# Kernel tuning notes

Hardware: AMD Instinct MI355X
Metric: run time of the kernel (lower is better)

Reference implementation:

```python
import jax, jax.numpy as jnp
import numpy as np

N_NODES = 100000
N_EDGES = 3200000


def gcn_conv(x, W, b, src, dst, n_nodes):
    """PyG GCNConv: self-loops, symmetric D^-1/2 A D^-1/2 norm, linear, bias."""
    loop = jnp.arange(n_nodes, dtype=src.dtype)
    s = jnp.concatenate([src, loop])  # [E+N]
    d = jnp.concatenate([dst, loop])  # [E+N]
    # degree computed at destination (col), edge_weight = 1
    deg = jax.ops.segment_sum(jnp.ones_like(d, dtype=x.dtype), d,
                              num_segments=n_nodes)
    dinv = jnp.where(deg > 0, jax.lax.rsqrt(deg), 0.0)
    norm = dinv[s] * dinv[d]  # [E+N]
    h = x @ W.T  # [N, out]
    msg = h[s] * norm[:, None]  # gather + scale, [E+N, out]
    out = jax.ops.segment_sum(msg, d, num_segments=n_nodes)  # scatter-add
    return out + b


def setup_inputs() -> dict:
    key = jax.random.key(0)
    k1, k2, k3, k4 = jax.random.split(key, 4)
    x = jax.random.normal(k1, (N_NODES, 2), dtype=jnp.float32)
    edge_index = jax.random.randint(k2, (2, N_EDGES), 0, N_NODES,
                                    dtype=jnp.int64)
    # Glorot-ish init for linear weights
    W1 = jax.random.normal(k3, (64, 2), dtype=jnp.float32) * 0.5
    b1 = jnp.zeros((64,), dtype=jnp.float32)
    W2 = jax.random.normal(k4, (2, 64), dtype=jnp.float32) * 0.125
    b2 = jnp.zeros((2,), dtype=jnp.float32)
    return {"x": x, "edge_index": edge_index, "W1": W1, "b1": b1,
            "W2": W2, "b2": b2}


def reference(x, edge_index, W1, b1, W2, b2):
    src, dst = edge_index[0], edge_index[1]
    h = gcn_conv(x, W1, b1, src, dst, N_NODES)
    h = jax.nn.relu(h)
    out = gcn_conv(h, W2, b2, src, dst, N_NODES)
    return out
```

## Files before the change

kernel.cpp:

```cpp
#include <hip/hip_runtime.h>

#define N_NODES 100000
#define SHIFT 8
#define BNODES 256
#define NB 391
#define CAP 9728
#define TILE 8192
#define SB 1024


__global__ __launch_bounds__(SB, 8) void k_sort(const int* __restrict__ src,
                                                const int* __restrict__ dst,
                                                int* claim,
                                                const int* __restrict__ pz,
                                                int* sg, int e) {
    __shared__ int hist[2 * NB];
    __shared__ int rank[2 * NB];
    __shared__ int addrbase[NB];
    __shared__ int partials[16];
    __shared__ int stage[TILE];
    __shared__ unsigned short binmap[TILE];

    const int t = threadIdx.x;
    const int base = blockIdx.x * TILE;
    const int n = min(TILE, e - base);
    const int goff = (t >> 9) * NB;

    for (int i = t; i < 2 * NB; i += SB) hist[i] = 0;
    __syncthreads();

    int recs[8];
    int bins[8];
    int* myh = hist + goff;
#pragma unroll
    for (int k = 0; k < 2; ++k) {
        int idx = base + (k * SB + t) * 4;
        if (idx + 3 < e) {
            int4 s4 = *(const int4*)(src + idx);
            int4 d4 = *(const int4*)(dst + idx);
            int ss[4] = {s4.x, s4.y, s4.z, s4.w};
            int dd[4] = {d4.x, d4.y, d4.z, d4.w};
#pragma unroll
            for (int j = 0; j < 4; ++j) {
                int b = dd[j] >> SHIFT;
                bins[4 * k + j] = b;
                recs[4 * k + j] = ss[j] | ((dd[j] & (BNODES - 1)) << 17);
                atomicAdd(&myh[b], 1);
            }
        } else {
#pragma unroll
            for (int j = 0; j < 4; ++j) {
                int i2 = idx + j;
                if (i2 < e) {
                    int d = dst[i2];
                    int b = d >> SHIFT;
                    bins[4 * k + j] = b;
                    recs[4 * k + j] = src[i2] | ((d & (BNODES - 1)) << 17);
                    atomicAdd(&myh[b], 1);
                } else {
                    bins[4 * k + j] = -1;
                }
            }
        }
    }
    __syncthreads();

    int c0 = 0, c1 = 0, c = 0;
    if (t < NB) {
        c0 = hist[t];
        c1 = hist[NB + t];
        c = c0 + c1;
    }
    int vs = c;
#pragma unroll
    for (int off = 1; off < 64; off <<= 1) {
        int w = __shfl_up(vs, off, 64);
        if ((t & 63) >= off) vs += w;
    }
    if ((t & 63) == 63) partials[t >> 6] = vs;
    __syncthreads();
    int add = 0;
    for (int w = 0; w < (t >> 6); ++w) add += partials[w];
    vs += add;
    int excl = vs - c;
    const int P = *pz;
    if (t < NB) {
        rank[t] = excl;
        rank[NB + t] = excl + c0;
        int rb = c ? (atomicAdd(&claim[t], c) - P) : 0;
        addrbase[t] = t * CAP + rb - excl;
    }
    __syncthreads();

    int* myr = rank + goff;
#pragma unroll
    for (int m = 0; m < 8; ++m) {
        int b = bins[m];
        if (b >= 0) {
            int pos = atomicAdd(&myr[b], 1);
            stage[pos] = recs[m];
            binmap[pos] = (unsigned short)b;
        }
    }
    __syncthreads();

    for (int i = t; i < n; i += SB) {
        sg[addrbase[binmap[i]] + i] = stage[i];
    }
}

__global__ __launch_bounds__(1024) void k_refine(const int* __restrict__ claim,
                                                 const int* __restrict__ pz,
                                                 const int* __restrict__ sg,
                                                 const float* __restrict__ x,
                                                 int* sg2, int* packed,
                                                 float2* u) {
    __shared__ int hist[4 * BNODES];
    __shared__ int rank[4 * BNODES];
    __shared__ int partials[4];
    const int t = threadIdx.x;
    const int b = blockIdx.x;
    const int* p = sg + b * CAP;
    const int len = claim[b] - *pz;
    const int g = t >> 8;

    int4 r[3];
#pragma unroll
    for (int k = 0; k < 3; ++k) {
        int idx = 4 * t + 4096 * k;
        int4 v = make_int4(-1, -1, -1, -1);
        if (idx + 3 < len) v = *(const int4*)(p + idx);
        else if (idx < len) {
            v.x = p[idx];
            if (idx + 1 < len) v.y = p[idx + 1];
            if (idx + 2 < len) v.z = p[idx + 2];
        }
        r[k] = v;
    }
    for (int i = t; i < 4 * BNODES; i += 1024) hist[i] = 0;
    __syncthreads();
    int* myh = hist + g * BNODES;
#pragma unroll
    for (int k = 0; k < 3; ++k) {
        if (r[k].x != -1) atomicAdd(&myh[((unsigned)r[k].x) >> 17], 1);
        if (r[k].y != -1) atomicAdd(&myh[((unsigned)r[k].y) >> 17], 1);
        if (r[k].z != -1) atomicAdd(&myh[((unsigned)r[k].z) >> 17], 1);
        if (r[k].w != -1) atomicAdd(&myh[((unsigned)r[k].w) >> 17], 1);
    }
    __syncthreads();

    int c4x = 0, c4y = 0, c4z = 0, c4w = 0, tot = 0;
    if (t < BNODES) {
        c4x = hist[t];
        c4y = hist[BNODES + t];
        c4z = hist[2 * BNODES + t];
        c4w = hist[3 * BNODES + t];
        tot = (c4x + c4y) + (c4z + c4w);
    }
    int vs = tot;
#pragma unroll
    for (int off = 1; off < 64; off <<= 1) {
        int w = __shfl_up(vs, off, 64);
        if ((t & 63) >= off) vs += w;
    }
    if ((t & 63) == 63 && t < BNODES) partials[t >> 6] = vs;
    __syncthreads();
    if (t < BNODES) {
        int add = 0;
        for (int w = 0; w < (t >> 6); ++w) add += partials[w];
        vs += add;
        int excl = vs - tot;
        int run = excl;
        rank[t] = run; run += c4x;
        rank[BNODES + t] = run; run += c4y;
        rank[2 * BNODES + t] = run; run += c4z;
        rank[3 * BNODES + t] = run;
        int node = b * BNODES + t;
        if (node < N_NODES) {
            packed[node] = (b * CAP + excl) | (tot << 22);
            float dv = rsqrtf((float)(tot + 1));
            float2 xv = ((const float2*)x)[node];
            u[node] = make_float2(dv * xv.x, dv * xv.y);
        }
    }
    __syncthreads();

    int* q = sg2 + b * CAP;
    int* myr = rank + g * BNODES;
#pragma unroll
    for (int k = 0; k < 3; ++k) {
        if (r[k].x != -1) q[atomicAdd(&myr[((unsigned)r[k].x) >> 17], 1)] = r[k].x & 0x1FFFF;
        if (r[k].y != -1) q[atomicAdd(&myr[((unsigned)r[k].y) >> 17], 1)] = r[k].y & 0x1FFFF;
        if (r[k].z != -1) q[atomicAdd(&myr[((unsigned)r[k].z) >> 17], 1)] = r[k].z & 0x1FFFF;
        if (r[k].w != -1) q[atomicAdd(&myr[((unsigned)r[k].w) >> 17], 1)] = r[k].w & 0x1FFFF;
    }
}

__global__ __launch_bounds__(256) void k_agg1(const int* __restrict__ sg2,
                                              const int* __restrict__ packed,
                                              const float2* __restrict__ u,
                                              const float* __restrict__ W1,
                                              const float* __restrict__ b1,
                                              const float* __restrict__ W2,
                                              float2* v) {
    __shared__ float sW1[128], sb1[64], sW2[128];
    int t = threadIdx.x;
    if (t < 128) { sW1[t] = W1[t]; sW2[t] = W2[t]; }
    else if (t < 192) sb1[t - 128] = b1[t - 128];
    __syncthreads();
    int n = blockIdx.x * 32 + (t >> 3);
    if (n >= N_NODES) return;
    int g = t & 7;
    int pk = packed[n];
    int s = pk & 0x3FFFFF;
    int cnt = ((unsigned)pk) >> 22;
    int e2 = s + cnt;
    float sx = 0.f, sy = 0.f;
    int i = s + g;
    for (; i + 24 < e2; i += 32) {
        float2 ga = u[sg2[i]];
        float2 gb = u[sg2[i + 8]];
        float2 gc = u[sg2[i + 16]];
        float2 gd = u[sg2[i + 24]];
        sx += (ga.x + gb.x) + (gc.x + gd.x);
        sy += (ga.y + gb.y) + (gc.y + gd.y);
    }
    for (; i + 8 < e2; i += 16) {
        float2 ga = u[sg2[i]];
        float2 gb = u[sg2[i + 8]];
        sx += ga.x + gb.x;
        sy += ga.y + gb.y;
    }
    if (i < e2) { float2 ga = u[sg2[i]]; sx += ga.x; sy += ga.y; }
    sx += __shfl_xor(sx, 1, 8); sy += __shfl_xor(sy, 1, 8);
    sx += __shfl_xor(sx, 2, 8); sy += __shfl_xor(sy, 2, 8);
    sx += __shfl_xor(sx, 4, 8); sy += __shfl_xor(sy, 4, 8);
    float dv = rsqrtf((float)(cnt + 1));
    float2 un = u[n];
    float a0 = dv * (sx + un.x), a1 = dv * (sy + un.y);
    float y0 = 0.f, y1 = 0.f;
#pragma unroll
    for (int k = 0; k < 8; ++k) {
        int j = g + 8 * k;
        float h = fmaxf(fmaf(sW1[2 * j], a0,
                        fmaf(sW1[2 * j + 1], a1, sb1[j])), 0.f);
        y0 = fmaf(sW2[j], h, y0);
        y1 = fmaf(sW2[64 + j], h, y1);
    }
    y0 += __shfl_xor(y0, 1, 8); y1 += __shfl_xor(y1, 1, 8);
    y0 += __shfl_xor(y0, 2, 8); y1 += __shfl_xor(y1, 2, 8);
    y0 += __shfl_xor(y0, 4, 8); y1 += __shfl_xor(y1, 4, 8);
    if (g == 0) v[n] = make_float2(dv * y0, dv * y1);
}

__global__ __launch_bounds__(256) void k_agg2(const int* __restrict__ sg2,
                                              const int* __restrict__ packed,
                                              const float2* __restrict__ v,
                                              const float* __restrict__ b2,
                                              float2* out) {
    int t = threadIdx.x;
    int n = blockIdx.x * 32 + (t >> 3);
    if (n >= N_NODES) return;
    int g = t & 7;
    int pk = packed[n];
    int s = pk & 0x3FFFFF;
    int cnt = ((unsigned)pk) >> 22;
    int e2 = s + cnt;
    float sx = 0.f, sy = 0.f;
    int i = s + g;
    for (; i + 24 < e2; i += 32) {
        float2 ga = v[sg2[i]];
        float2 gb = v[sg2[i + 8]];
        float2 gc = v[sg2[i + 16]];
        float2 gd = v[sg2[i + 24]];
        sx += (ga.x + gb.x) + (gc.x + gd.x);
        sy += (ga.y + gb.y) + (gc.y + gd.y);
    }
    for (; i + 8 < e2; i += 16) {
        float2 ga = v[sg2[i]];
        float2 gb = v[sg2[i + 8]];
        sx += ga.x + gb.x;
        sy += ga.y + gb.y;
    }
    if (i < e2) { float2 ga = v[sg2[i]]; sx += ga.x; sy += ga.y; }
    sx += __shfl_xor(sx, 1, 8); sy += __shfl_xor(sy, 1, 8);
    sx += __shfl_xor(sx, 2, 8); sy += __shfl_xor(sy, 2, 8);
    sx += __shfl_xor(sx, 4, 8); sy += __shfl_xor(sy, 4, 8);
    if (g == 0) {
        float dv = rsqrtf((float)(cnt + 1));
        float2 vn = v[n];
        out[n] = make_float2(fmaf(dv, sx + vn.x, b2[0]),
                             fmaf(dv, sy + vn.y, b2[1]));
    }
}

extern "C" void kernel_launch(void* const* d_in, const int* in_sizes, int n_in,
                              void* d_out, int out_size, void* d_ws, size_t ws_size,
                              hipStream_t stream) {
    const float* x  = (const float*)d_in[0];
    const int* ei   = (const int*)d_in[1];
    const float* W1 = (const float*)d_in[2];
    const float* b1 = (const float*)d_in[3];
    const float* W2 = (const float*)d_in[4];
    const float* b2 = (const float*)d_in[5];

    int e = in_sizes[1] / 2;
    const int* src = ei;
    const int* dst = ei + e;

    int* ws      = (int*)d_ws;
    int* claim   = ws;
    int* pz      = ws + NB;
    int* sg      = ws + 392;
    int* sg2     = sg + NB * CAP;
    int* packed  = sg2 + NB * CAP;
    float2* u    = (float2*)(packed + N_NODES);
    float2* v    = u + N_NODES;
    float2* outp = (float2*)d_out;

    const int gA = (N_NODES + 31) / 32;
    k_sort  <<<(e + TILE - 1) / TILE, SB, 0, stream>>>(src, dst, claim, pz, sg, e);
    k_refine<<<NB, 1024, 0, stream>>>(claim, pz, sg, x, sg2, packed, u);
    k_agg1  <<<gA, 256, 0, stream>>>(sg2, packed, u, W1, b1, W2, v);
    k_agg2  <<<gA, 256, 0, stream>>>(sg2, packed, v, b2, outp);
}
```

Before: 148.3 us.

## Replace per-node CSR refinement with per-bucket shared-memory float atomic aggregation

Removes the second-level sort that produced a per-node CSR (sg2/packed). A small degree kernel now builds dinv and u, and each layer's aggregation runs per 256-node bucket: every block gathers its bucket's edges and accumulates source features into shared-memory float atomics, then applies the MLP or bias per node. This drops the sg2 write and the packed index reads. In exchange it adds two extra passes over the bucketed edge list, puts heavy contention on shared-memory float atomics, and makes the summation order nondeterministic. Only 391 blocks of 1024 threads carry the gathers.

```diff
diff --git a/kernel.cpp b/kernel.cpp
--- a/kernel.cpp
+++ b/kernel.cpp
@@ -109,188 +109,169 @@
     }
 }
 
-__global__ __launch_bounds__(1024) void k_refine(const int* __restrict__ claim,
-                                                 const int* __restrict__ pz,
-                                                 const int* __restrict__ sg,
-                                                 const float* __restrict__ x,
-                                                 int* sg2, int* packed,
-                                                 float2* u) {
-    __shared__ int hist[4 * BNODES];
-    __shared__ int rank[4 * BNODES];
-    __shared__ int partials[4];
+__global__ __launch_bounds__(1024) void k_deg(const int* __restrict__ claim,
+                                              const int* __restrict__ pz,
+                                              const int* __restrict__ sg,
+                                              const float* __restrict__ x,
+                                              float2* __restrict__ u,
+                                              float* __restrict__ dinv) {
+    __shared__ int hist[2 * BNODES];
     const int t = threadIdx.x;
     const int b = blockIdx.x;
     const int* p = sg + b * CAP;
     const int len = claim[b] - *pz;
-    const int g = t >> 8;
+    if (t < 2 * BNODES) hist[t] = 0;
+    __syncthreads();
+    int* myh = hist + (t >> 9) * BNODES;
+    for (int i = t; i < len; i += 1024) {
+        atomicAdd(&myh[((unsigned)p[i]) >> 17], 1);
+    }
+    __syncthreads();
+    if (t < BNODES) {
+        int node = b * BNODES + t;
+        if (node < N_NODES) {
+            int tot = hist[t] + hist[BNODES + t];
+            float dv = rsqrtf((float)(tot + 1));
+            dinv[node] = dv;
+            float2 xv = ((const float2*)x)[node];
+            u[node] = make_float2(dv * xv.x, dv * xv.y);
+        }
+    }
+}
+
+__global__ __launch_bounds__(1024) void k_l1(const int* __restrict__ claim,
+                                             const int* __restrict__ pz,
+                                             const int* __restrict__ sg,
+                                             const float* __restrict__ dinv,
+                                             const float2* __restrict__ u,
+                                             const float* __restrict__ W1,
+                                             const float* __restrict__ b1,
+                                             const float* __restrict__ W2,
+                                             float2* __restrict__ v) {
+    __shared__ float ax[BNODES], ay[BNODES];
+    __shared__ float sW1[128], sb1[64], sW2[128];
+    const int t = threadIdx.x;
+    const int b = blockIdx.x;
+    const int* p = sg + b * CAP;
+    const int len = claim[b] - *pz;
+
+    if (t < 128) { sW1[t] = W1[t]; sW2[t] = W2[t]; }
+    if (t >= 128 && t < 192) sb1[t - 128] = b1[t - 128];
+    if (t < BNODES) { ax[t] = 0.f; ay[t] = 0.f; }
 
     int4 r[3];
 #pragma unroll
     for (int k = 0; k < 3; ++k) {
         int idx = 4 * t + 4096 * k;
-        int4 v = make_int4(-1, -1, -1, -1);
-        if (idx + 3 < len) v = *(const int4*)(p + idx);
+        int4 vv = make_int4(-1, -1, -1, -1);
+        if (idx + 3 < len) vv = *(const int4*)(p + idx);
         else if (idx < len) {
-            v.x = p[idx];
-            if (idx + 1 < len) v.y = p[idx + 1];
-            if (idx + 2 < len) v.z = p[idx + 2];
-        }
-        r[k] = v;
-    }
-    for (int i = t; i < 4 * BNODES; i += 1024) hist[i] = 0;
-    __syncthreads();
-    int* myh = hist + g * BNODES;
+            vv.x = p[idx];
+            if (idx + 1 < len) vv.y = p[idx + 1];
+            if (idx + 2 < len) vv.z = p[idx + 2];
+        }
+        r[k] = vv;
+    }
+    __syncthreads();
+
 #pragma unroll
     for (int k = 0; k < 3; ++k) {
-        if (r[k].x != -1) atomicAdd(&myh[((unsigned)r[k].x) >> 17], 1);
-        if (r[k].y != -1) atomicAdd(&myh[((unsigned)r[k].y) >> 17], 1);
-        if (r[k].z != -1) atomicAdd(&myh[((unsigned)r[k].z) >> 17], 1);
-        if (r[k].w != -1) atomicAdd(&myh[((unsigned)r[k].w) >> 17], 1);
-    }
-    __syncthreads();
-
-    int c4x = 0, c4y = 0, c4z = 0, c4w = 0, tot = 0;
+        const bool v0 = r[k].x != -1, v1 = r[k].y != -1,
+                   v2 = r[k].z != -1, v3 = r[k].w != -1;
+        float2 g0, g1, g2, g3;
+        if (v0) g0 = u[r[k].x & 0x1FFFF];
+        if (v1) g1 = u[r[k].y & 0x1FFFF];
+        if (v2) g2 = u[r[k].z & 0x1FFFF];
+        if (v3) g3 = u[r[k].w & 0x1FFFF];
+        if (v0) { atomicAdd(&ax[((unsigned)r[k].x) >> 17], g0.x);
+                  atomicAdd(&ay[((unsigned)r[k].x) >> 17], g0.y); }
+        if (v1) { atomicAdd(&ax[((unsigned)r[k].y) >> 17], g1.x);
+                  atomicAdd(&ay[((unsigned)r[k].y) >> 17], g1.y); }
+        if (v2) { atomicAdd(&ax[((unsigned)r[k].z) >> 17], g2.x);
+                  atomicAdd(&ay[((unsigned)r[k].z) >> 17], g2.y); }
+        if (v3) { atomicAdd(&ax[((unsigned)r[k].w) >> 17], g3.x);
+                  atomicAdd(&ay[((unsigned)r[k].w) >> 17], g3.y); }
+    }
+    __syncthreads();
+
     if (t < BNODES) {
-        c4x = hist[t];
-        c4y = hist[BNODES + t];
-        c4z = hist[2 * BNODES + t];
-        c4w = hist[3 * BNODES + t];
-        tot = (c4x + c4y) + (c4z + c4w);
-    }
-    int vs = tot;
-#pragma unroll
-    for (int off = 1; off < 64; off <<= 1) {
-        int w = __shfl_up(vs, off, 64);
-        if ((t & 63) >= off) vs += w;
-    }
-    if ((t & 63) == 63 && t < BNODES) partials[t >> 6] = vs;
-    __syncthreads();
-    if (t < BNODES) {
-        int add = 0;
-        for (int w = 0; w < (t >> 6); ++w) add += partials[w];
-        vs += add;
-        int excl = vs - tot;
-        int run = excl;
-        rank[t] = run; run += c4x;
-        rank[BNODES + t] = run; run += c4y;
-        rank[2 * BNODES + t] = run; run += c4z;
-        rank[3 * BNODES + t] = run;
         int node = b * BNODES + t;
         if (node < N_NODES) {
-            packed[node] = (b * CAP + excl) | (tot << 22);
-            float dv = rsqrtf((float)(tot + 1));
-            float2 xv = ((const float2*)x)[node];
-            u[node] = make_float2(dv * xv.x, dv * xv.y);
-        }
-    }
-    __syncthreads();
-
-    int* q = sg2 + b * CAP;
-    int* myr = rank + g * BNODES;
+            float dv = dinv[node];
+            float2 uo = u[node];
+            float a0 = dv * (ax[t] + uo.x);
+            float a1 = dv * (ay[t] + uo.y);
+            float y0 = 0.f, y1 = 0.f;
+#pragma unroll 8
+            for (int j = 0; j < 64; ++j) {
+                float h = fmaxf(fmaf(sW1[2 * j], a0,
+                                fmaf(sW1[2 * j + 1], a1, sb1[j])), 0.f);
+                y0 = fmaf(sW2[j], h, y0);
+                y1 = fmaf(sW2[64 + j], h, y1);
+            }
+            v[node] = make_float2(dv * y0, dv * y1);
+        }
+    }
+}
+
+__global__ __launch_bounds__(1024) void k_l2(const int* __restrict__ claim,
+                                             const int* __restrict__ pz,
+                                             const int* __restrict__ sg,
+                                             const float* __restrict__ dinv,
+                                             const float2* __restrict__ v,
+                                             const float* __restrict__ b2,
+                                             float2* __restrict__ out) {
+    __shared__ float ax[BNODES], ay[BNODES];
+    const int t = threadIdx.x;
+    const int b = blockIdx.x;
+    const int* p = sg + b * CAP;
+    const int len = claim[b] - *pz;
+
+    if (t < BNODES) { ax[t] = 0.f; ay[t] = 0.f; }
+
+    int4 r[3];
 #pragma unroll
     for (int k = 0; k < 3; ++k) {
-        if (r[k].x != -1) q[atomicAdd(&myr[((unsigned)r[k].x) >> 17], 1)] = r[k].x & 0x1FFFF;
-        if (r[k].y != -1) q[atomicAdd(&myr[((unsigned)r[k].y) >> 17], 1)] = r[k].y & 0x1FFFF;
-        if (r[k].z != -1) q[atomicAdd(&myr[((unsigned)r[k].z) >> 17], 1)] = r[k].z & 0x1FFFF;
-        if (r[k].w != -1) q[atomicAdd(&myr[((unsigned)r[k].w) >> 17], 1)] = r[k].w & 0x1FFFF;
-    }
-}
-
-__global__ __launch_bounds__(256) void k_agg1(const int* __restrict__ sg2,
-                                              const int* __restrict__ packed,
-                                              const float2* __restrict__ u,
-                                              const float* __restrict__ W1,
-                                              const float* __restrict__ b1,
-                                              const float* __restrict__ W2,
-                                              float2* v) {
-    __shared__ float sW1[128], sb1[64], sW2[128];
-    int t = threadIdx.x;
-    if (t < 128) { sW1[t] = W1[t]; sW2[t] = W2[t]; }
-    else if (t < 192) sb1[t - 128] = b1[t - 128];
-    __syncthreads();
-    int n = blockIdx.x * 32 + (t >> 3);
-    if (n >= N_NODES) return;
-    int g = t & 7;
-    int pk = packed[n];
-    int s = pk & 0x3FFFFF;
-    int cnt = ((unsigned)pk) >> 22;
-    int e2 = s + cnt;
-    float sx = 0.f, sy = 0.f;
-    int i = s + g;
-    for (; i + 24 < e2; i += 32) {
-        float2 ga = u[sg2[i]];
-        float2 gb = u[sg2[i + 8]];
-        float2 gc = u[sg2[i + 16]];
-        float2 gd = u[sg2[i + 24]];
-        sx += (ga.x + gb.x) + (gc.x + gd.x);
-        sy += (ga.y + gb.y) + (gc.y + gd.y);
-    }
-    for (; i + 8 < e2; i += 16) {
-        float2 ga = u[sg2[i]];
-        float2 gb = u[sg2[i + 8]];
-        sx += ga.x + gb.x;
-        sy += ga.y + gb.y;
-    }
-    if (i < e2) { float2 ga = u[sg2[i]]; sx += ga.x; sy += ga.y; }
-    sx += __shfl_xor(sx, 1, 8); sy += __shfl_xor(sy, 1, 8);
-    sx += __shfl_xor(sx, 2, 8); sy += __shfl_xor(sy, 2, 8);
-    sx += __shfl_xor(sx, 4, 8); sy += __shfl_xor(sy, 4, 8);
-    float dv = rsqrtf((float)(cnt + 1));
-    float2 un = u[n];
-    float a0 = dv * (sx + un.x), a1 = dv * (sy + un.y);
-    float y0 = 0.f, y1 = 0.f;
-#pragma unroll
-    for (int k = 0; k < 8; ++k) {
-        int j = g + 8 * k;
-        float h = fmaxf(fmaf(sW1[2 * j], a0,
-                        fmaf(sW1[2 * j + 1], a1, sb1[j])), 0.f);
-        y0 = fmaf(sW2[j], h, y0);
-        y1 = fmaf(sW2[64 + j], h, y1);
-    }
-    y0 += __shfl_xor(y0, 1, 8); y1 += __shfl_xor(y1, 1, 8);
-    y0 += __shfl_xor(y0, 2, 8); y1 += __shfl_xor(y1, 2, 8);
-    y0 += __shfl_xor(y0, 4, 8); y1 += __shfl_xor(y1, 4, 8);
-    if (g == 0) v[n] = make_float2(dv * y0, dv * y1);
-}
-
-__global__ __launch_bounds__(256) void k_agg2(const int* __restrict__ sg2,
-                                              const int* __restrict__ packed,
-                                              const float2* __restrict__ v,
-                                              const float* __restrict__ b2,
-                                              float2* out) {
-    int t = threadIdx.x;
-    int n = blockIdx.x * 32 + (t >> 3);
-    if (n >= N_NODES) return;
-    int g = t & 7;
-    int pk = packed[n];
-    int s = pk & 0x3FFFFF;
-    int cnt = ((unsigned)pk) >> 22;
-    int e2 = s + cnt;
-    float sx = 0.f, sy = 0.f;
-    int i = s + g;
-    for (; i + 24 < e2; i += 32) {
-        float2 ga = v[sg2[i]];
-        float2 gb = v[sg2[i + 8]];
-        float2 gc = v[sg2[i + 16]];
-        float2 gd = v[sg2[i + 24]];
-        sx += (ga.x + gb.x) + (gc.x + gd.x);
-        sy += (ga.y + gb.y) + (gc.y + gd.y);
-    }
-    for (; i + 8 < e2; i += 16) {
-        float2 ga = v[sg2[i]];
-        float2 gb = v[sg2[i + 8]];
-        sx += ga.x + gb.x;
-        sy += ga.y + gb.y;
-    }
-    if (i < e2) { float2 ga = v[sg2[i]]; sx += ga.x; sy += ga.y; }
-    sx += __shfl_xor(sx, 1, 8); sy += __shfl_xor(sy, 1, 8);
-    sx += __shfl_xor(sx, 2, 8); sy += __shfl_xor(sy, 2, 8);
-    sx += __shfl_xor(sx, 4, 8); sy += __shfl_xor(sy, 4, 8);
-    if (g == 0) {
-        float dv = rsqrtf((float)(cnt + 1));
-        float2 vn = v[n];
-        out[n] = make_float2(fmaf(dv, sx + vn.x, b2[0]),
-                             fmaf(dv, sy + vn.y, b2[1]));
+        int idx = 4 * t + 4096 * k;
+        int4 vv = make_int4(-1, -1, -1, -1);
+        if (idx + 3 < len) vv = *(const int4*)(p + idx);
+        else if (idx < len) {
+            vv.x = p[idx];
+            if (idx + 1 < len) vv.y = p[idx + 1];
+            if (idx + 2 < len) vv.z = p[idx + 2];
+        }
+        r[k] = vv;
+    }
+    __syncthreads();
+
+#pragma unroll
+    for (int k = 0; k < 3; ++k) {
+        const bool v0 = r[k].x != -1, v1 = r[k].y != -1,
+                   v2 = r[k].z != -1, v3 = r[k].w != -1;
+        float2 g0, g1, g2, g3;
+        if (v0) g0 = v[r[k].x & 0x1FFFF];
+        if (v1) g1 = v[r[k].y & 0x1FFFF];
+        if (v2) g2 = v[r[k].z & 0x1FFFF];
+        if (v3) g3 = v[r[k].w & 0x1FFFF];
+        if (v0) { atomicAdd(&ax[((unsigned)r[k].x) >> 17], g0.x);
+                  atomicAdd(&ay[((unsigned)r[k].x) >> 17], g0.y); }
+        if (v1) { atomicAdd(&ax[((unsigned)r[k].y) >> 17], g1.x);
+                  atomicAdd(&ay[((unsigned)r[k].y) >> 17], g1.y); }
+        if (v2) { atomicAdd(&ax[((unsigned)r[k].z) >> 17], g2.x);
+                  atomicAdd(&ay[((unsigned)r[k].z) >> 17], g2.y); }
+        if (v3) { atomicAdd(&ax[((unsigned)r[k].w) >> 17], g3.x);
+                  atomicAdd(&ay[((unsigned)r[k].w) >> 17], g3.y); }
+    }
+    __syncthreads();
+
+    if (t < BNODES) {
+        int node = b * BNODES + t;
+        if (node < N_NODES) {
+            float dv = dinv[node];
+            float2 vo = v[node];
+            out[node] = make_float2(fmaf(dv, ax[t] + vo.x, b2[0]),
+                                    fmaf(dv, ay[t] + vo.y, b2[1]));
+        }
     }
 }
 
@@ -312,15 +293,13 @@
     int* claim   = ws;
     int* pz      = ws + NB;
     int* sg      = ws + 392;
-    int* sg2     = sg + NB * CAP;
-    int* packed  = sg2 + NB * CAP;
-    float2* u    = (float2*)(packed + N_NODES);
+    float2* u    = (float2*)(sg + NB * CAP);
     float2* v    = u + N_NODES;
+    float* dinv  = (float*)(v + N_NODES);
     float2* outp = (float2*)d_out;
 
-    const int gA = (N_NODES + 31) / 32;
-    k_sort  <<<(e + TILE - 1) / TILE, SB, 0, stream>>>(src, dst, claim, pz, sg, e);
-    k_refine<<<NB, 1024, 0, stream>>>(claim, pz, sg, x, sg2, packed, u);
-    k_agg1  <<<gA, 256, 0, stream>>>(sg2, packed, u, W1, b1, W2, v);
-    k_agg2  <<<gA, 256, 0, stream>>>(sg2, packed, v, b2, outp);
-}
+    k_sort<<<(e + TILE - 1) / TILE, SB, 0, stream>>>(src, dst, claim, pz, sg, e);
+    k_deg <<<NB, 1024, 0, stream>>>(claim, pz, sg, x, u, dinv);
+    k_l1  <<<NB, 1024, 0, stream>>>(claim, pz, sg, dinv, u, W1, b1, W2, v);
+    k_l2  <<<NB, 1024, 0, stream>>>(claim, pz, sg, dinv, v, b2, outp);
+}
```

Measured after the change: 193.6 us. 30.5% more time.
